# Optimization experiments

Hardware: AMD Instinct MI355X
Metric: run time of the kernel (lower is better)

The kernel has to match this reference:

```python
import jax, jax.numpy as jnp
import numpy as np

B, S, D = 2, 2048, 2048
H, KV, HD = 32, 8, 64
REP = H // KV  # 4


def setup_inputs() -> dict:
    key = jax.random.key(0)
    ks = jax.random.split(key, 5)
    x = jax.random.normal(ks[0], (B, S, D), jnp.float32)
    # Llama rope frequencies: theta=10000, pairs of adjacent dims
    inv_freq = 1.0 / (10000.0 ** (np.arange(0, HD, 2, dtype=np.float64) / HD))  # [HD/2]
    ang = np.outer(np.arange(S, dtype=np.float64), inv_freq)  # [S, HD/2]
    freqs_cis = jnp.asarray(np.stack([np.cos(ang), np.sin(ang)], axis=-1), jnp.float32)  # [S, HD/2, 2]
    wq = jax.random.normal(ks[1], (H * HD, D), jnp.float32) * 0.02
    wk = jax.random.normal(ks[2], (KV * HD, D), jnp.float32) * 0.02
    wv = jax.random.normal(ks[3], (KV * HD, D), jnp.float32) * 0.02
    wo = jax.random.normal(ks[4], (D, H * HD), jnp.float32) * 0.02
    return {"x": x, "freqs_cis": freqs_cis, "wq": wq, "wk": wk, "wv": wv, "wo": wo}


def _apply_rope(t, cos, sin):
    # t: [B,S,nh,HD]; cos/sin: [S,HD/2]; complex multiply on adjacent pairs
    b, s, nh, hd = t.shape
    t2 = t.reshape(b, s, nh, hd // 2, 2)
    tr, ti = t2[..., 0], t2[..., 1]
    c = cos[None, :, None, :]
    sn = sin[None, :, None, :]
    out = jnp.stack([tr * c - ti * sn, tr * sn + ti * c], axis=-1)
    return out.reshape(b, s, nh, hd)


def reference(x, freqs_cis, wq, wk, wv, wo):
    # QKV projections (torch Linear: y = x @ W.T)
    q = jnp.einsum('bsd,ed->bse', x, wq).reshape(B, S, H, HD)
    k = jnp.einsum('bsd,ed->bse', x, wk).reshape(B, S, KV, HD)
    v = jnp.einsum('bsd,ed->bse', x, wv).reshape(B, S, KV, HD)
    cos, sin = freqs_cis[..., 0], freqs_cis[..., 1]
    q = _apply_rope(q, cos, sin)
    k = _apply_rope(k, cos, sin)
    # GQA without materializing repeated K/V: group query heads by KV head
    qg = q.reshape(B, S, KV, REP, HD)
    scale = 1.0 / jnp.sqrt(jnp.asarray(HD, q.dtype))
    scores = jnp.einsum('bsgrd,btgd->bgrst', qg, k) * scale  # [B,KV,REP,S,S]
    causal = jnp.tril(jnp.ones((S, S), bool))
    scores = jnp.where(causal, scores, -jnp.inf)
    p = jax.nn.softmax(scores, axis=-1)
    o = jnp.einsum('bgrst,btgd->bsgrd', p, v).reshape(B, S, H * HD)
    return jnp.einsum('bse,de->bsd', o, wo)
```

## Files before the change

kernel.cpp:

```cpp
#include <hip/hip_runtime.h>
#include <cstdint>
#include <cstddef>

#define B_ 2
#define S_ 2048
#define D_ 2048
#define H_ 32
#define KV_ 8
#define HD_ 64
#define M_ (B_*S_)
#define EQ_ (H_*HD_)
#define EK_ (KV_*HD_)

typedef unsigned short u16;
typedef __attribute__((ext_vector_type(8))) short s16x8;
typedef __attribute__((ext_vector_type(4))) float f32x4;

#define QSCALE 0.18033688011112042f
#define EXPOFF 15.869645449778564f

#if __has_builtin(__builtin_amdgcn_exp2f)
#define EXP2(x) __builtin_amdgcn_exp2f(x)
#else
#define EXP2(x) __expf((x) * 0.6931471805599453f)
#endif

__device__ __forceinline__ u16 f2bf(float f) {
  unsigned u = __float_as_uint(f);
  u += 0x7fffu + ((u >> 16) & 1u);
  return (u16)(u >> 16);
}
__device__ __forceinline__ unsigned pk2(float a, float b) {
  unsigned ua = __float_as_uint(a) + 0x8000u;
  unsigned ub = __float_as_uint(b) + 0x8000u;
  return __builtin_amdgcn_perm(ub, ua, 0x07060302);
}
__device__ __forceinline__ f32x4 mfma16(s16x8 a, s16x8 b, f32x4 c) {
  return __builtin_amdgcn_mfma_f32_16x16x32_bf16(a, b, c, 0, 0, 0);
}
__device__ __forceinline__ void gl_lds16(const void* g, void* l) {
  __builtin_amdgcn_global_load_lds(
      (const __attribute__((address_space(1))) void*)g,
      (__attribute__((address_space(3))) void*)l, 16, 0, 0);
}

__global__ void cast_all(const float4* __restrict__ x, const float4* __restrict__ wq,
                         const float4* __restrict__ wk, const float4* __restrict__ wv,
                         const float4* __restrict__ wo, ushort4* __restrict__ dst) {
  int i = blockIdx.x * 256 + threadIdx.x;
  const float4* src; int off;
  if (i < 2097152)      { src = x;  off = i; }
  else if (i < 3145728) { src = wq; off = i - 2097152; }
  else if (i < 3407872) { src = wk; off = i - 3145728; }
  else if (i < 3670016) { src = wv; off = i - 3407872; }
  else                  { src = wo; off = i - 3670016; }
  float4 v = src[off];
  ushort4 r;
  r.x = f2bf(v.x); r.y = f2bf(v.y); r.z = f2bf(v.z); r.w = f2bf(v.w);
  dst[i] = r;
}

__global__ __launch_bounds__(256)
void gemm_qkv(const u16* __restrict__ A, const u16* __restrict__ Bw,
              u16* __restrict__ qb, u16* __restrict__ kb, u16* __restrict__ vtb,
              const float* __restrict__ fc) {
  __shared__ __align__(16) u16 As[2][128 * 32];
  __shared__ __align__(16) u16 Bs[2][96 * 32];
  const int tid  = threadIdx.x;
  const int lane = tid & 63;
  const int wave = tid >> 6;
  const int m0 = blockIdx.y * 128;
  const int n0 = blockIdx.x * 96;
  const int wm = (wave >> 1) * 64;
  const int wn = (wave & 1) * 48;
  const int l15 = lane & 15;
  const int quad = lane >> 4;

  const int ca0 = tid,      ra0 = ca0 >> 2, pa0 = ca0 & 3;
  const int ca1 = tid + 256, ra1 = ca1 >> 2, pa1 = ca1 & 3;
  const int cb0 = tid,      rb0 = cb0 >> 2, pb0 = cb0 & 3;
  const int cb1 = tid + 256, rb1 = cb1 >> 2, pb1 = cb1 & 3;
  const u16* Ap0 = A + (size_t)(m0 + ra0) * D_ + (pa0 ^ ((ra0 >> 1) & 3)) * 8;
  const u16* Ap1 = A + (size_t)(m0 + ra1) * D_ + (pa1 ^ ((ra1 >> 1) & 3)) * 8;
  const u16* Bp0 = Bw + (size_t)(n0 + rb0) * D_ + (pb0 ^ ((rb0 >> 1) & 3)) * 8;
  const u16* Bp1 = Bw + (size_t)(n0 + rb1) * D_ + (pb1 ^ ((rb1 >> 1) & 3)) * 8;
  const bool doB1 = (tid < 128);

  f32x4 acc[4][3] = {};

  gl_lds16(Ap0, &As[0][ca0 * 8]);
  gl_lds16(Ap1, &As[0][ca1 * 8]);
  gl_lds16(Bp0, &Bs[0][cb0 * 8]);
  if (doB1) gl_lds16(Bp1, &Bs[0][cb1 * 8]);
  __syncthreads();

  for (int ks = 0; ks < 64; ++ks) {
    if (ks + 1 < 64) {
      const int nb = (ks + 1) & 1;
      const int ko = (ks + 1) * 32;
      gl_lds16(Ap0 + ko, &As[nb][ca0 * 8]);
      gl_lds16(Ap1 + ko, &As[nb][ca1 * 8]);
      gl_lds16(Bp0 + ko, &Bs[nb][cb0 * 8]);
      if (doB1) gl_lds16(Bp1 + ko, &Bs[nb][cb1 * 8]);
    }

    const u16* as = &As[ks & 1][0];
    const u16* bs = &Bs[ks & 1][0];
    s16x8 af[4], bfr[3];
    #pragma unroll
    for (int mi = 0; mi < 4; ++mi) {
      int row = wm + mi * 16 + l15;
      af[mi] = *(const s16x8*)&as[row * 32 + (quad ^ ((row >> 1) & 3)) * 8];
    }
    #pragma unroll
    for (int ni = 0; ni < 3; ++ni) {
      int row = wn + ni * 16 + l15;
      bfr[ni] = *(const s16x8*)&bs[row * 32 + (quad ^ ((row >> 1) & 3)) * 8];
    }
    #pragma unroll
    for (int mi = 0; mi < 4; ++mi)
      #pragma unroll
      for (int ni = 0; ni < 3; ++ni)
        acc[mi][ni] = mfma16(af[mi], bfr[ni], acc[mi][ni]);

    __syncthreads();
  }

  const float sg = (l15 & 1) ? 1.f : -1.f;
  #pragma unroll
  for (int mi = 0; mi < 4; ++mi) {
    #pragma unroll
    for (int ni = 0; ni < 3; ++ni) {
      const int col = n0 + wn + ni * 16 + l15;
      if (col < 2560) {
        const bool isQ = (col < 2048);
        u16* dst = isQ ? qb : kb;
        const int ncol0 = isQ ? 0 : 2048;
        const int ndim  = isQ ? EQ_ : EK_;
        const float scale = isQ ? QSCALE : 1.0f;
        const int ip = (col & 63) >> 1;
        #pragma unroll
        for (int r = 0; r < 4; ++r) {
          int row = m0 + wm + mi * 16 + quad * 4 + r;
          const float* fr = fc + (size_t)(row & (S_ - 1)) * 64;
          float c  = fr[ip * 2];
          float sn = fr[ip * 2 + 1];
          float v = acc[mi][ni][r];
          float p = __shfl_xor(v, 1, 64);
          float o = (v * c + sg * (p * sn)) * scale;
          dst[(size_t)row * ndim + col - ncol0] = f2bf(o);
        }
      } else {
        const int vcol = col - 2560;
        uint2 w;
        w.x = pk2(acc[mi][ni][0], acc[mi][ni][1]);
        w.y = pk2(acc[mi][ni][2], acc[mi][ni][3]);
        *(uint2*)(vtb + (size_t)vcol * M_ + m0 + wm + mi * 16 + quad * 4) = w;
      }
    }
  }
}

__global__ __launch_bounds__(256)
void gemm_o(const u16* __restrict__ A, const u16* __restrict__ Bw, float* __restrict__ C,
            int Ndim, int Kdim) {
  __shared__ __align__(16) u16 As[2][64 * 32];
  __shared__ __align__(16) u16 Bs[2][128 * 32];
  const int tid  = threadIdx.x;
  const int lane = tid & 63;
  const int wave = tid >> 6;
  const int m0 = blockIdx.y * 64;
  const int n0 = blockIdx.x * 128;
  const int wm = (wave >> 1) * 32;
  const int wn = (wave & 1) * 64;
  const int l15 = lane & 15;
  const int quad = lane >> 4;

  const int ca0 = tid,      ra0 = ca0 >> 2, pa0 = ca0 & 3;
  const int cb0 = tid,      rb0 = cb0 >> 2, pb0 = cb0 & 3;
  const int cb1 = tid + 256, rb1 = cb1 >> 2, pb1 = cb1 & 3;
  const u16* Ap0 = A + (size_t)(m0 + ra0) * Kdim + (pa0 ^ ((ra0 >> 1) & 3)) * 8;
  const u16* Bp0 = Bw + (size_t)(n0 + rb0) * Kdim + (pb0 ^ ((rb0 >> 1) & 3)) * 8;
  const u16* Bp1 = Bw + (size_t)(n0 + rb1) * Kdim + (pb1 ^ ((rb1 >> 1) & 3)) * 8;

  f32x4 acc[2][4] = {};

  const int nsteps = Kdim >> 5;

  gl_lds16(Ap0, &As[0][ca0 * 8]);
  gl_lds16(Bp0, &Bs[0][cb0 * 8]);
  gl_lds16(Bp1, &Bs[0][cb1 * 8]);
  __syncthreads();

  for (int ks = 0; ks < nsteps; ++ks) {
    if (ks + 1 < nsteps) {
      const int nb = (ks + 1) & 1;
      const int ko = (ks + 1) * 32;
      gl_lds16(Ap0 + ko, &As[nb][ca0 * 8]);
      gl_lds16(Bp0 + ko, &Bs[nb][cb0 * 8]);
      gl_lds16(Bp1 + ko, &Bs[nb][cb1 * 8]);
    }

    const u16* as = &As[ks & 1][0];
    const u16* bs = &Bs[ks & 1][0];
    s16x8 af[2], bfr[4];
    #pragma unroll
    for (int mi = 0; mi < 2; ++mi) {
      int row = wm + mi * 16 + l15;
      af[mi] = *(const s16x8*)&as[row * 32 + (quad ^ ((row >> 1) & 3)) * 8];
    }
    #pragma unroll
    for (int ni = 0; ni < 4; ++ni) {
      int row = wn + ni * 16 + l15;
      bfr[ni] = *(const s16x8*)&bs[row * 32 + (quad ^ ((row >> 1) & 3)) * 8];
    }
    #pragma unroll
    for (int mi = 0; mi < 2; ++mi)
      #pragma unroll
      for (int ni = 0; ni < 4; ++ni)
        acc[mi][ni] = mfma16(af[mi], bfr[ni], acc[mi][ni]);

    __syncthreads();
  }

  #pragma unroll
  for (int mi = 0; mi < 2; ++mi) {
    #pragma unroll
    for (int r = 0; r < 4; ++r) {
      int row = m0 + wm + mi * 16 + quad * 4 + r;
      size_t base = (size_t)row * Ndim + n0 + wn;
      #pragma unroll
      for (int ni = 0; ni < 4; ++ni)
        C[base + ni * 16 + l15] = acc[mi][ni][r];
    }
  }
}

__global__ __launch_bounds__(256, 4)
void flash_attn(const u16* __restrict__ qb, const u16* __restrict__ kb,
                const u16* __restrict__ vtb, u16* __restrict__ ob) {
  const int bx = blockIdx.x;
  const int h  = blockIdx.y;
  const int b  = blockIdx.z;
  const int g  = h >> 2;
  const int tid  = threadIdx.x;
  const int lane = tid & 63;
  const int wave = tid >> 6;
  const int l15  = lane & 15;
  const int quad = lane >> 4;
  const int kq   = quad * 8;

  const int Tlo = bx, Thi = 31 - bx;
  const int n_lo = Tlo + 1, n_hi = Thi + 1;
  const int rL = Tlo * 64 + wave * 16;
  const int rH = Thi * 64 + wave * 16;
  const int rowL = rL + l15;
  const int rowH = rH + l15;

  __shared__ __align__(16) u16 Ks[2][8 * 512];
  __shared__ __align__(16) u16 Vs[8 * 512];
  __shared__ __align__(16) u16 Pl[4][2][16 * 64];

  char* PbL = (char*)&Pl[wave][0][0];
  char* PbH = (char*)&Pl[wave][1][0];
  const int pm = (l15 & 7) << 4;

  const u16* qpL = qb + (size_t)(b * S_ + rL + l15) * EQ_ + h * HD_;
  const u16* qpH = qb + (size_t)(b * S_ + rH + l15) * EQ_ + h * HD_;
  s16x8 qL0 = *(const s16x8*)(qpL + kq);
  s16x8 qL1 = *(const s16x8*)(qpL + 32 + kq);
  s16x8 qH0 = *(const s16x8*)(qpH + kq);
  s16x8 qH1 = *(const s16x8*)(qpH + 32 + kq);

  f32x4 OL[4] = {}, OH[4] = {};
  float sumL = 0.f, sumH = 0.f;

  const int sw = wave & 1;
  const bool doK = (wave < 2);

  const u16* stbase;
  size_t     tstride;
  if (doK) {
    stbase  = kb + (size_t)(b * S_ + lane) * EK_ + g * HD_ + sw * 32;
    tstride = (size_t)64 * EK_;
  } else {
    stbase  = vtb + (size_t)(g * HD_ + lane) * M_ + b * S_ + sw * 32;
    tstride = 64;
  }
  const int ldoff = sw * 4 * 512 + lane * 8;

  if (doK) {
    #pragma unroll
    for (int r = 0; r < 4; ++r)
      gl_lds16(stbase + r * 8, &Ks[0][ldoff + r * 512]);
  }
  __syncthreads();

  for (int kt = 0; kt < n_hi; ++kt) {
    const int t0 = kt * 64;
    const u16* kcur = &Ks[kt & 1][0];

    if (doK) {
      if (kt + 1 < n_hi) {
        const u16* src = stbase + (size_t)(kt + 1) * tstride;
        u16* dst = &Ks[(kt + 1) & 1][ldoff];
        #pragma unroll
        for (int r = 0; r < 4; ++r)
          gl_lds16(src + r * 8, dst + r * 512);
      }
    } else {
      const u16* src = stbase + (size_t)kt * tstride;
      #pragma unroll
      for (int r = 0; r < 4; ++r)
        gl_lds16(src + r * 8, &Vs[ldoff + r * 512]);
    }

    const bool do_lo = (kt < n_lo);
    const bool mH = (kt == n_hi - 1);
    const bool mL = (kt == n_lo - 1);

    #pragma unroll
    for (int ts = 0; ts < 4; ++ts) {
      s16x8 k0 = *(const s16x8*)&kcur[quad * 512 + (ts * 16 + l15) * 8];
      s16x8 k1 = *(const s16x8*)&kcur[(4 + quad) * 512 + (ts * 16 + l15) * 8];
      const int tb = t0 + ts * 16 + quad * 4;
      {
        f32x4 s = {};
        s = mfma16(k0, qH0, s);
        s = mfma16(k1, qH1, s);
        if (mH) {
          #pragma unroll
          for (int r = 0; r < 4; ++r) if (tb + r > rowH) s[r] = -1e30f;
        }
        float p0 = EXP2(s[0] - EXPOFF), p1 = EXP2(s[1] - EXPOFF);
        float p2 = EXP2(s[2] - EXPOFF), p3 = EXP2(s[3] - EXPOFF);
        sumH += (p0 + p1) + (p2 + p3);
        uint2 w; w.x = pk2(p0, p1); w.y = pk2(p2, p3);
        *(uint2*)(PbH + l15 * 128 + ((ts * 32 + quad * 8) ^ pm)) = w;
      }
      if (do_lo) {
        f32x4 s = {};
        s = mfma16(k0, qL0, s);
        s = mfma16(k1, qL1, s);
        if (mL) {
          #pragma unroll
          for (int r = 0; r < 4; ++r) if (tb + r > rowL) s[r] = -1e30f;
        }
        float p0 = EXP2(s[0] - EXPOFF), p1 = EXP2(s[1] - EXPOFF);
        float p2 = EXP2(s[2] - EXPOFF), p3 = EXP2(s[3] - EXPOFF);
        sumL += (p0 + p1) + (p2 + p3);
        uint2 w; w.x = pk2(p0, p1); w.y = pk2(p2, p3);
        *(uint2*)(PbL + l15 * 128 + ((ts * 32 + quad * 8) ^ pm)) = w;
      }
    }

    s16x8 pH0 = *(const s16x8*)(PbH + l15 * 128 + ((quad * 16) ^ pm));
    s16x8 pH1 = *(const s16x8*)(PbH + l15 * 128 + ((64 + quad * 16) ^ pm));
    s16x8 pL0 = {}, pL1 = {};
    if (do_lo) {
      pL0 = *(const s16x8*)(PbL + l15 * 128 + ((quad * 16) ^ pm));
      pL1 = *(const s16x8*)(PbL + l15 * 128 + ((64 + quad * 16) ^ pm));
    }

    __syncthreads();

    #pragma unroll
    for (int df = 0; df < 4; ++df) {
      s16x8 v0 = *(const s16x8*)&Vs[quad * 512 + (df * 16 + l15) * 8];
      s16x8 v1 = *(const s16x8*)&Vs[(4 + quad) * 512 + (df * 16 + l15) * 8];
      OH[df] = mfma16(v1, pH1, mfma16(v0, pH0, OH[df]));
      if (do_lo) OL[df] = mfma16(v1, pL1, mfma16(v0, pL0, OL[df]));
    }

    __syncthreads();
  }

  sumH += __shfl_xor(sumH, 16, 64); sumH += __shfl_xor(sumH, 32, 64);
  sumL += __shfl_xor(sumL, 16, 64); sumL += __shfl_xor(sumL, 32, 64);
  float invH = 1.f / sumH, invL = 1.f / sumL;

  {
    u16* op = ob + (size_t)(b * S_ + rowH) * EQ_ + h * HD_;
    #pragma unroll
    for (int df = 0; df < 4; ++df) {
      uint2 w;
      w.x = pk2(OH[df][0] * invH, OH[df][1] * invH);
      w.y = pk2(OH[df][2] * invH, OH[df][3] * invH);
      *(uint2*)(op + df * 16 + quad * 4) = w;
    }
  }
  {
    u16* op = ob + (size_t)(b * S_ + rowL) * EQ_ + h * HD_;
    #pragma unroll
    for (int df = 0; df < 4; ++df) {
      uint2 w;
      w.x = pk2(OL[df][0] * invL, OL[df][1] * invL);
      w.y = pk2(OL[df][2] * invL, OL[df][3] * invL);
      *(uint2*)(op + df * 16 + quad * 4) = w;
    }
  }
}

extern "C" void kernel_launch(void* const* d_in, const int* in_sizes, int n_in,
                              void* d_out, int out_size, void* d_ws, size_t ws_size,
                              hipStream_t stream) {
  (void)in_sizes; (void)n_in; (void)out_size; (void)ws_size;
  const float* x  = (const float*)d_in[0];
  const float* fc = (const float*)d_in[1];
  const float* wq = (const float*)d_in[2];
  const float* wk = (const float*)d_in[3];
  const float* wv = (const float*)d_in[4];
  const float* wo = (const float*)d_in[5];
  float* out = (float*)d_out;
  char* ws = (char*)d_ws;

  u16* xb  = (u16*)(ws);
  u16* wqb = (u16*)(ws + 16777216);
  u16* wob = (u16*)(ws + 29360128);
  u16* qb  = (u16*)(ws + 37748736);
  u16* kb  = (u16*)(ws + 54525952);
  u16* vtb = (u16*)(ws + 58720256);
  u16* ob  = (u16*)(ws + 62914560);

  cast_all<<<18432, 256, 0, stream>>>((const float4*)x, (const float4*)wq,
                                      (const float4*)wk, (const float4*)wv,
                                      (const float4*)wo, (ushort4*)ws);

  gemm_qkv<<<dim3(32, 32), 256, 0, stream>>>(xb, wqb, qb, kb, vtb, fc);

  flash_attn<<<dim3(16, 32, 2), 256, 0, stream>>>(qb, kb, vtb, ob);

  gemm_o<<<dim3(16, 64), 256, 0, stream>>>(ob, wob, out, D_, EQ_);
}
```

Before: 308.6 us.

## Double-buffer V tiles and drop mid-iteration barrier in attention loop

V tiles now get the same two-buffer prefetch as K. All four waves load the next K or V tile while the current one is consumed, which removes the barrier between the P computation and the PV MFMAs. The per-wave P scratch is shared between the high and low row blocks, and K fragments are hoisted into registers so they can be reused across both blocks. This trades more LDS for V and more live registers against less waiting on synchronisation and on V loads. Reusing the P buffer without a barrier depends on wave-local ordering of LDS reads and writes.

```diff
diff --git a/kernel.cpp b/kernel.cpp
--- a/kernel.cpp
+++ b/kernel.cpp
@@ -258,11 +258,10 @@
   const int rowH = rH + l15;
 
   __shared__ __align__(16) u16 Ks[2][8 * 512];
-  __shared__ __align__(16) u16 Vs[8 * 512];
-  __shared__ __align__(16) u16 Pl[4][2][16 * 64];
-
-  char* PbL = (char*)&Pl[wave][0][0];
-  char* PbH = (char*)&Pl[wave][1][0];
+  __shared__ __align__(16) u16 Vs[2][8 * 512];
+  __shared__ __align__(16) u16 Pl[4][16 * 64];
+
+  char* Pb = (char*)&Pl[wave][0];
   const int pm = (l15 & 7) << 4;
 
   const u16* qpL = qb + (size_t)(b * S_ + rL + l15) * EQ_ + h * HD_;
@@ -288,60 +287,65 @@
     tstride = 64;
   }
   const int ldoff = sw * 4 * 512 + lane * 8;
-
-  if (doK) {
-    #pragma unroll
-    for (int r = 0; r < 4; ++r)
-      gl_lds16(stbase + r * 8, &Ks[0][ldoff + r * 512]);
-  }
+  u16* mybuf0 = (doK ? &Ks[0][0] : &Vs[0][0]) + ldoff;
+  u16* mybuf1 = (doK ? &Ks[1][0] : &Vs[1][0]) + ldoff;
+
+  #pragma unroll
+  for (int r = 0; r < 4; ++r)
+    gl_lds16(stbase + r * 8, mybuf0 + r * 512);
   __syncthreads();
 
   for (int kt = 0; kt < n_hi; ++kt) {
     const int t0 = kt * 64;
     const u16* kcur = &Ks[kt & 1][0];
-
-    if (doK) {
-      if (kt + 1 < n_hi) {
-        const u16* src = stbase + (size_t)(kt + 1) * tstride;
-        u16* dst = &Ks[(kt + 1) & 1][ldoff];
-        #pragma unroll
-        for (int r = 0; r < 4; ++r)
-          gl_lds16(src + r * 8, dst + r * 512);
-      }
-    } else {
-      const u16* src = stbase + (size_t)kt * tstride;
+    const u16* vcur = &Vs[kt & 1][0];
+
+    if (kt + 1 < n_hi) {
+      const u16* src = stbase + (size_t)(kt + 1) * tstride;
+      u16* dst = ((kt + 1) & 1) ? mybuf1 : mybuf0;
       #pragma unroll
       for (int r = 0; r < 4; ++r)
-        gl_lds16(src + r * 8, &Vs[ldoff + r * 512]);
+        gl_lds16(src + r * 8, dst + r * 512);
     }
 
     const bool do_lo = (kt < n_lo);
     const bool mH = (kt == n_hi - 1);
     const bool mL = (kt == n_lo - 1);
 
+    s16x8 kk0[4], kk1[4];
     #pragma unroll
     for (int ts = 0; ts < 4; ++ts) {
-      s16x8 k0 = *(const s16x8*)&kcur[quad * 512 + (ts * 16 + l15) * 8];
-      s16x8 k1 = *(const s16x8*)&kcur[(4 + quad) * 512 + (ts * 16 + l15) * 8];
+      kk0[ts] = *(const s16x8*)&kcur[quad * 512 + (ts * 16 + l15) * 8];
+      kk1[ts] = *(const s16x8*)&kcur[(4 + quad) * 512 + (ts * 16 + l15) * 8];
+    }
+
+    #pragma unroll
+    for (int ts = 0; ts < 4; ++ts) {
       const int tb = t0 + ts * 16 + quad * 4;
-      {
+      f32x4 s = {};
+      s = mfma16(kk0[ts], qH0, s);
+      s = mfma16(kk1[ts], qH1, s);
+      if (mH) {
+        #pragma unroll
+        for (int r = 0; r < 4; ++r) if (tb + r > rowH) s[r] = -1e30f;
+      }
+      float p0 = EXP2(s[0] - EXPOFF), p1 = EXP2(s[1] - EXPOFF);
+      float p2 = EXP2(s[2] - EXPOFF), p3 = EXP2(s[3] - EXPOFF);
+      sumH += (p0 + p1) + (p2 + p3);
+      uint2 w; w.x = pk2(p0, p1); w.y = pk2(p2, p3);
+      *(uint2*)(Pb + l15 * 128 + ((ts * 32 + quad * 8) ^ pm)) = w;
+    }
+    s16x8 pH0 = *(const s16x8*)(Pb + l15 * 128 + ((quad * 16) ^ pm));
+    s16x8 pH1 = *(const s16x8*)(Pb + l15 * 128 + ((64 + quad * 16) ^ pm));
+
+    s16x8 pL0 = {}, pL1 = {};
+    if (do_lo) {
+      #pragma unroll
+      for (int ts = 0; ts < 4; ++ts) {
+        const int tb = t0 + ts * 16 + quad * 4;
         f32x4 s = {};
-        s = mfma16(k0, qH0, s);
-        s = mfma16(k1, qH1, s);
-        if (mH) {
-          #pragma unroll
-          for (int r = 0; r < 4; ++r) if (tb + r > rowH) s[r] = -1e30f;
-        }
-        float p0 = EXP2(s[0] - EXPOFF), p1 = EXP2(s[1] - EXPOFF);
-        float p2 = EXP2(s[2] - EXPOFF), p3 = EXP2(s[3] - EXPOFF);
-        sumH += (p0 + p1) + (p2 + p3);
-        uint2 w; w.x = pk2(p0, p1); w.y = pk2(p2, p3);
-        *(uint2*)(PbH + l15 * 128 + ((ts * 32 + quad * 8) ^ pm)) = w;
-      }
-      if (do_lo) {
-        f32x4 s = {};
-        s = mfma16(k0, qL0, s);
-        s = mfma16(k1, qL1, s);
+        s = mfma16(kk0[ts], qL0, s);
+        s = mfma16(kk1[ts], qL1, s);
         if (mL) {
           #pragma unroll
           for (int r = 0; r < 4; ++r) if (tb + r > rowL) s[r] = -1e30f;
@@ -350,24 +354,16 @@
         float p2 = EXP2(s[2] - EXPOFF), p3 = EXP2(s[3] - EXPOFF);
         sumL += (p0 + p1) + (p2 + p3);
         uint2 w; w.x = pk2(p0, p1); w.y = pk2(p2, p3);
-        *(uint2*)(PbL + l15 * 128 + ((ts * 32 + quad * 8) ^ pm)) = w;
+        *(uint2*)(Pb + l15 * 128 + ((ts * 32 + quad * 8) ^ pm)) = w;
       }
-    }
-
-    s16x8 pH0 = *(const s16x8*)(PbH + l15 * 128 + ((quad * 16) ^ pm));
-    s16x8 pH1 = *(const s16x8*)(PbH + l15 * 128 + ((64 + quad * 16) ^ pm));
-    s16x8 pL0 = {}, pL1 = {};
-    if (do_lo) {
-      pL0 = *(const s16x8*)(PbL + l15 * 128 + ((quad * 16) ^ pm));
-      pL1 = *(const s16x8*)(PbL + l15 * 128 + ((64 + quad * 16) ^ pm));
-    }
-
-    __syncthreads();
+      pL0 = *(const s16x8*)(Pb + l15 * 128 + ((quad * 16) ^ pm));
+      pL1 = *(const s16x8*)(Pb + l15 * 128 + ((64 + quad * 16) ^ pm));
+    }
 
     #pragma unroll
     for (int df = 0; df < 4; ++df) {
-      s16x8 v0 = *(const s16x8*)&Vs[quad * 512 + (df * 16 + l15) * 8];
-      s16x8 v1 = *(const s16x8*)&Vs[(4 + quad) * 512 + (df * 16 + l15) * 8];
+      s16x8 v0 = *(const s16x8*)&vcur[quad * 512 + (df * 16 + l15) * 8];
+      s16x8 v1 = *(const s16x8*)&vcur[(4 + quad) * 512 + (df * 16 + l15) * 8];
       OH[df] = mfma16(v1, pH1, mfma16(v0, pH0, OH[df]));
       if (do_lo) OL[df] = mfma16(v1, pL1, mfma16(v0, pL0, OL[df]));
     }
```

Measured after the change: 310.1 us. About the same (+0.5%).
